# Performance work log

Hardware: AMD Instinct MI355X
Metric: run time of the kernel (lower is better)

Reference implementation:

```python
import jax, jax.numpy as jnp
import numpy as np

NNZ = 819200
BATCH = 4096          # sp_x.dense_shape[0]; static num_segments
VOCAB = 1000000       # input_size
K = 16                # num_latent_variables


def setup_inputs() -> dict:
    key = jax.random.key(0)
    k1, k2, k3, k4 = jax.random.split(key, 4)
    indices = jax.random.randint(k1, (NNZ,), 0, VOCAB, dtype=jnp.int32)
    batch_ids = jnp.sort(jax.random.randint(k2, (NNZ,), 0, BATCH, dtype=jnp.int32))
    values = jax.random.normal(k3, (NNZ,), dtype=jnp.float32)
    weight = jax.random.normal(k4, (VOCAB, K), dtype=jnp.float32) * 0.05
    return {"indices": indices, "batch_ids": batch_ids, "values": values, "weight": weight}


def reference(indices, batch_ids, values, weight):
    # v = embedding_lookup(weight, indices) * values  -> [nnz, K]
    v_times_x = weight[indices] * values[:, None]
    # sum_i v_i x_i per example -> [BATCH, K]
    all_crosses = jax.ops.segment_sum(v_times_x, batch_ids, num_segments=BATCH)
    all_crosses_squared = jnp.sum(all_crosses * all_crosses, axis=1)  # (sum v x)^2
    # self-cross subtraction: sum_i (v_i x_i)^2 per example
    self_crosses = jnp.sum(
        jax.ops.segment_sum(v_times_x * v_times_x, batch_ids, num_segments=BATCH), axis=1
    )
    outputs = all_crosses_squared - self_crosses  # [BATCH]
    # linear activation (None); pad_empty_outputs handled by num_segments=BATCH
    return outputs.reshape(-1, 1)
```

## Files before the change

### kernel.cpp

```cpp
#include <hip/hip_runtime.h>


#define FM_K 16

__global__ __launch_bounds__(256) void FactorizationMachine_75144747810873_kernel(
    const int* __restrict__ indices,
    const int* __restrict__ batch_ids,
    const float* __restrict__ values,
    const float* __restrict__ weight,
    float* __restrict__ out,
    int nnz, int nbatch)
{
    const int tid  = threadIdx.x;
    const int wave = tid >> 6;
    const int lane = tid & 63;
    const int kq   = lane & 3;
    const int sub  = lane >> 2;
    const int wip  = wave & 1;
    const int pair = wave >> 1;

    const int b = blockIdx.x * 2 + pair;
    const bool bvalid = (b < nbatch);

    __shared__ float4 accbuf[4][4];
    __shared__ float  selfbuf[4];

    float4 acc  = make_float4(0.f, 0.f, 0.f, 0.f);
    float  self = 0.f;

    if (bvalid) {
        int lo = 0, hi = nnz;
        while (lo < hi) {
            int mid = (lo + hi) >> 1;
            if (batch_ids[mid] < b) lo = mid + 1; else hi = mid;
        }
        const int start = lo;
        hi = nnz;
        while (lo < hi) {
            int mid = (lo + hi) >> 1;
            if (batch_ids[mid] < b + 1) lo = mid + 1; else hi = mid;
        }
        const int end = lo;

        int e = start + sub + wip * 16;
        bool valid = (e < end);
        int   idx = 0;
        float x   = 0.f;
        if (valid) { idx = indices[e]; x = values[e]; }

        while (valid) {
            const int  e2 = e + 32;
            const bool v2 = (e2 < end);
            int   idx2 = 0;
            float x2   = 0.f;
            if (v2) { idx2 = indices[e2]; x2 = values[e2]; }

            const float4 w4 = *reinterpret_cast<const float4*>(
                weight + (long long)idx * FM_K + kq * 4);
            const float4 wx = make_float4(w4.x * x, w4.y * x, w4.z * x, w4.w * x);
            acc.x += wx.x; acc.y += wx.y; acc.z += wx.z; acc.w += wx.w;
            self  += wx.x * wx.x + wx.y * wx.y + wx.z * wx.z + wx.w * wx.w;

            e = e2; valid = v2; idx = idx2; x = x2;
        }
    }

    for (int off = 4; off < 64; off <<= 1) {
        acc.x += __shfl_xor(acc.x, off);
        acc.y += __shfl_xor(acc.y, off);
        acc.z += __shfl_xor(acc.z, off);
        acc.w += __shfl_xor(acc.w, off);
    }
    for (int off = 1; off < 64; off <<= 1)
        self += __shfl_xor(self, off);

    if (lane < 4)  accbuf[wave][lane] = acc;
    if (lane == 0) selfbuf[wave] = self;
    __syncthreads();

    if (wip == 0 && bvalid) {
        const float4 a0 = accbuf[wave][kq];
        const float4 a1 = accbuf[wave + 1][kq];
        const float4 s  = make_float4(a0.x + a1.x, a0.y + a1.y,
                                      a0.z + a1.z, a0.w + a1.w);
        float sq = s.x * s.x + s.y * s.y + s.z * s.z + s.w * s.w;
        sq += __shfl_xor(sq, 1);
        sq += __shfl_xor(sq, 2);
        const float selftot = selfbuf[wave] + selfbuf[wave + 1];
        if (lane == 0) out[b] = sq - selftot;
    }
}

extern "C" void kernel_launch(void* const* d_in, const int* in_sizes, int n_in,
                              void* d_out, int out_size, void* d_ws, size_t ws_size,
                              hipStream_t stream) {
    const int*   indices   = (const int*)d_in[0];
    const int*   batch_ids = (const int*)d_in[1];
    const float* values    = (const float*)d_in[2];
    const float* weight    = (const float*)d_in[3];
    float*       out       = (float*)d_out;
    const int nnz = in_sizes[0];

    const int grid = (out_size + 1) / 2;
    FactorizationMachine_75144747810873_kernel<<<grid, 256, 0, stream>>>(
        indices, batch_ids, values, weight, out, nnz, out_size);
}
```

Measured before the change: 120.7 us.

## Precompute segment splits in a separate kernel and use one block per batch row

Adds a pre-pass kernel that writes CSR-style segment boundaries into workspace, so the main kernel no longer does two binary searches per batch row. The main kernel now assigns one 256-thread block per row with all four waves sharing the segment, and batches four index/value loads per wave to keep more gathers in flight. It also switches weight addressing to 32-bit arithmetic. The cost is an extra kernel launch and a pass over batch_ids, and the grid doubles while each block gets less work per wave for the roughly 200 nnz per row.

```diff
diff --git a/kernel.cpp b/kernel.cpp
--- a/kernel.cpp
+++ b/kernel.cpp
@@ -3,90 +3,97 @@
 
 #define FM_K 16
 
+__global__ __launch_bounds__(256) void fm_splits_kernel(
+    const int* __restrict__ batch_ids,
+    int* __restrict__ splits,
+    int nnz, int nbatch)
+{
+    const int e = blockIdx.x * 256 + threadIdx.x;
+    if (e > nnz) return;
+    if (e == 0) {
+        const int cur = batch_ids[0];
+        for (int b = 0; b <= cur; ++b) splits[b] = 0;
+    } else if (e == nnz) {
+        const int prev = batch_ids[nnz - 1];
+        for (int b = prev + 1; b <= nbatch; ++b) splits[b] = nnz;
+    } else {
+        const int prev = batch_ids[e - 1];
+        const int cur  = batch_ids[e];
+        for (int b = prev + 1; b <= cur; ++b) splits[b] = e;
+    }
+}
+
 __global__ __launch_bounds__(256) void FactorizationMachine_75144747810873_kernel(
     const int* __restrict__ indices,
-    const int* __restrict__ batch_ids,
     const float* __restrict__ values,
     const float* __restrict__ weight,
-    float* __restrict__ out,
-    int nnz, int nbatch)
+    const int* __restrict__ splits,
+    float* __restrict__ out)
 {
     const int tid  = threadIdx.x;
     const int wave = tid >> 6;
     const int lane = tid & 63;
     const int kq   = lane & 3;
     const int sub  = lane >> 2;
-    const int wip  = wave & 1;
-    const int pair = wave >> 1;
 
-    const int b = blockIdx.x * 2 + pair;
-    const bool bvalid = (b < nbatch);
-
-    __shared__ float4 accbuf[4][4];
-    __shared__ float  selfbuf[4];
+    const int b     = blockIdx.x;
+    const int start = splits[b];
+    const int end   = splits[b + 1];
 
     float4 acc  = make_float4(0.f, 0.f, 0.f, 0.f);
     float  self = 0.f;
 
-    if (bvalid) {
-        int lo = 0, hi = nnz;
-        while (lo < hi) {
-            int mid = (lo + hi) >> 1;
-            if (batch_ids[mid] < b) lo = mid + 1; else hi = mid;
+    for (int base = start + 16 * wave; base < end; base += 256) {
+        int   idxv[4];
+        float xv[4];
+#pragma unroll
+        for (int u = 0; u < 4; ++u) {
+            const int  e = base + 64 * u + sub;
+            const bool v = (e < end);
+            idxv[u] = v ? indices[e] : 0;
+            xv[u]   = v ? values[e]  : 0.f;
         }
-        const int start = lo;
-        hi = nnz;
-        while (lo < hi) {
-            int mid = (lo + hi) >> 1;
-            if (batch_ids[mid] < b + 1) lo = mid + 1; else hi = mid;
-        }
-        const int end = lo;
-
-        int e = start + sub + wip * 16;
-        bool valid = (e < end);
-        int   idx = 0;
-        float x   = 0.f;
-        if (valid) { idx = indices[e]; x = values[e]; }
-
-        while (valid) {
-            const int  e2 = e + 32;
-            const bool v2 = (e2 < end);
-            int   idx2 = 0;
-            float x2   = 0.f;
-            if (v2) { idx2 = indices[e2]; x2 = values[e2]; }
-
+#pragma unroll
+        for (int u = 0; u < 4; ++u) {
             const float4 w4 = *reinterpret_cast<const float4*>(
-                weight + (long long)idx * FM_K + kq * 4);
+                weight + idxv[u] * FM_K + kq * 4);
+            const float x = xv[u];
             const float4 wx = make_float4(w4.x * x, w4.y * x, w4.z * x, w4.w * x);
             acc.x += wx.x; acc.y += wx.y; acc.z += wx.z; acc.w += wx.w;
             self  += wx.x * wx.x + wx.y * wx.y + wx.z * wx.z + wx.w * wx.w;
-
-            e = e2; valid = v2; idx = idx2; x = x2;
         }
     }
 
+#pragma unroll
     for (int off = 4; off < 64; off <<= 1) {
         acc.x += __shfl_xor(acc.x, off);
         acc.y += __shfl_xor(acc.y, off);
         acc.z += __shfl_xor(acc.z, off);
         acc.w += __shfl_xor(acc.w, off);
     }
+#pragma unroll
     for (int off = 1; off < 64; off <<= 1)
         self += __shfl_xor(self, off);
 
-    if (lane < 4)  accbuf[wave][lane] = acc;
+    __shared__ float4 accbuf[4][4];
+    __shared__ float  selfbuf[4];
+    if (sub == 0)  accbuf[wave][kq] = acc;
     if (lane == 0) selfbuf[wave] = self;
     __syncthreads();
 
-    if (wip == 0 && bvalid) {
-        const float4 a0 = accbuf[wave][kq];
-        const float4 a1 = accbuf[wave + 1][kq];
-        const float4 s  = make_float4(a0.x + a1.x, a0.y + a1.y,
-                                      a0.z + a1.z, a0.w + a1.w);
+    if (wave == 0) {
+        const float4 a0 = accbuf[0][kq];
+        const float4 a1 = accbuf[1][kq];
+        const float4 a2 = accbuf[2][kq];
+        const float4 a3 = accbuf[3][kq];
+        const float4 s  = make_float4(a0.x + a1.x + a2.x + a3.x,
+                                      a0.y + a1.y + a2.y + a3.y,
+                                      a0.z + a1.z + a2.z + a3.z,
+                                      a0.w + a1.w + a2.w + a3.w);
         float sq = s.x * s.x + s.y * s.y + s.z * s.z + s.w * s.w;
         sq += __shfl_xor(sq, 1);
         sq += __shfl_xor(sq, 2);
-        const float selftot = selfbuf[wave] + selfbuf[wave + 1];
+        const float selftot = selfbuf[0] + selfbuf[1] + selfbuf[2] + selfbuf[3];
         if (lane == 0) out[b] = sq - selftot;
     }
 }
@@ -99,9 +106,11 @@
     const float* values    = (const float*)d_in[2];
     const float* weight    = (const float*)d_in[3];
     float*       out       = (float*)d_out;
+    int*         splits    = (int*)d_ws;
     const int nnz = in_sizes[0];
 
-    const int grid = (out_size + 1) / 2;
-    FactorizationMachine_75144747810873_kernel<<<grid, 256, 0, stream>>>(
-        indices, batch_ids, values, weight, out, nnz, out_size);
+    fm_splits_kernel<<<(nnz + 1 + 255) / 256, 256, 0, stream>>>(
+        batch_ids, splits, nnz, out_size);
+    FactorizationMachine_75144747810873_kernel<<<out_size, 256, 0, stream>>>(
+        indices, values, weight, splits, out);
 }
```

Result: faster. 111.3 us (-7.8%).
